# Kernel tuning notes

Measured on AMD Instinct MI355X. Metric: run time of the kernel, lower is better.

The kernel has to match this reference:

```python
import jax, jax.numpy as jnp
import numpy as np

DIM = 96
HEADS = 3
WIN = (8, 8)
B_ = 4096
N = WIN[0] * WIN[1]


def _rel_pos_index(win):
    ch, cw = np.arange(win[0]), np.arange(win[1])
    coords = np.stack(np.meshgrid(ch, cw, indexing='ij'))  # [2, Wh, Ww]
    flat = coords.reshape(2, -1)
    rel = flat[:, :, None] - flat[:, None, :]  # [2, N, N]
    rel = rel.transpose(1, 2, 0).copy()
    rel[:, :, 0] += win[0] - 1
    rel[:, :, 1] += win[1] - 1
    rel[:, :, 0] *= 2 * win[1] - 1
    return jnp.asarray(rel.sum(-1), dtype=jnp.int32)  # [N, N]


def setup_inputs() -> dict:
    key = jax.random.key(0)
    ks = jax.random.split(key, 16)
    C = DIM
    T = (2 * WIN[0] - 1) * (2 * WIN[1] - 1)  # 225
    d = {
        'input_x': jax.random.normal(ks[0], (B_, N, C), jnp.float32),
        'state_x': jax.random.normal(ks[1], (B_, N, C), jnp.float32),
        'Ws': jax.random.normal(ks[2], (4 * C, C), jnp.float32) * 0.02,
        'bs': jnp.zeros((4 * C,), jnp.float32),
        'We': jax.random.normal(ks[3], (4 * C, C), jnp.float32) * 0.02,
        'be': jnp.zeros((4 * C,), jnp.float32),
        'tbl_cv': jax.random.normal(ks[4], (T, HEADS), jnp.float32) * 0.02,
        'tbl_sv': jax.random.normal(ks[5], (T, HEADS), jnp.float32) * 0.02,
        'tbl_ch': jax.random.normal(ks[6], (T, HEADS), jnp.float32) * 0.02,
        'tbl_sh': jax.random.normal(ks[7], (T, HEADS), jnp.float32) * 0.02,
        'Wpv': jax.random.normal(ks[8], (C, 2 * C), jnp.float32) * 0.02,
        'bpv': jnp.zeros((C,), jnp.float32),
        'Wph': jax.random.normal(ks[9], (C, 2 * C), jnp.float32) * 0.02,
        'bph': jnp.zeros((C,), jnp.float32),
        'rel_idx': _rel_pos_index(WIN),
    }
    return d


def _split4(x, W, b, B, n, H, hd):
    # Linear -> [4, B, H, n, hd]
    y = (x @ W.T + b).reshape(B, n, 4, H, hd)
    return jnp.transpose(y, (2, 0, 3, 1, 4))


def reference(input_x, state_x, Ws, bs, We, be, tbl_cv, tbl_sv, tbl_ch, tbl_sh,
              Wpv, bpv, Wph, bph, rel_idx):
    B, n, C = input_x.shape
    H = HEADS
    hd = C // H
    scale = hd ** (-0.5)

    sl = _split4(state_x, Ws, bs, B, n, H, hd)
    el = _split4(input_x, We, be, B, n, H, hd)
    ks_, vs, qsv, qsh = sl[0], sl[1], sl[2], sl[3]
    ke, ve, qev, qeh = el[0], el[1], el[2], el[3]

    def bias(tbl):
        # gather [N,N,H] -> [1,H,N,N]
        return jnp.transpose(tbl[rel_idx], (2, 0, 1))[None]

    # NOTE: faithful to source: self_attn_v is UNscaled, self_attn_h is double-scaled
    attn_cv = jax.nn.softmax(scale * jnp.einsum('bhnd,bhmd->bhnm', qsv, ks_) + bias(tbl_cv), axis=-1)
    attn_sv = jax.nn.softmax(jnp.einsum('bhnd,bhmd->bhnm', qev, ke) + bias(tbl_sv), axis=-1)
    attn_ch = jax.nn.softmax(scale * jnp.einsum('bhnd,bhmd->bhnm', qeh, ke) + bias(tbl_ch), axis=-1)
    attn_sh = jax.nn.softmax((scale * scale) * jnp.einsum('bhnd,bhmd->bhnm', qsh, ks_) + bias(tbl_sh), axis=-1)

    def merge(attn, v):
        return jnp.einsum('bhnm,bhmd->bnhd', attn, v).reshape(B, n, C)

    cross_x_v = merge(attn_cv, vs)
    self_x_v = merge(attn_sv, ve)
    cross_x_h = merge(attn_ch, ve)
    self_x_h = merge(attn_sh, vs)

    out = jnp.concatenate((cross_x_v, self_x_v), axis=2) @ Wpv.T + bpv
    state = jnp.concatenate((cross_x_h, self_x_h), axis=2) @ Wph.T + bph
    return out, state
```

## Files before the change

kernel.cpp:

```cpp
#include <hip/hip_runtime.h>

#define NB 4096
#define NSEQ 64
#define CDIM 96
#define NH 3

typedef __attribute__((ext_vector_type(8))) short bf16x8;
typedef __attribute__((ext_vector_type(4))) float f32x4;
typedef unsigned short u16;

#define MFMA16 __builtin_amdgcn_mfma_f32_16x16x32_bf16

__device__ __forceinline__ u16 f2bf(float f) {
  unsigned u = __builtin_bit_cast(unsigned, f);
  u += 0x7FFFu + ((u >> 16) & 1u);
  return (u16)(u >> 16);
}

__global__ __launch_bounds__(256) void bias_pre_kernel(
    const float* __restrict__ tcv, const float* __restrict__ tsv,
    const float* __restrict__ tch, const float* __restrict__ tsh,
    const int* __restrict__ rel, float* __restrict__ biasF) {
  int idx = blockIdx.x * 256 + threadIdx.x;
  if (idx >= 4 * 3 * 16 * 64) return;
  int t = idx / (3 * 16 * 64);
  int r0 = idx % (3 * 16 * 64);
  int h = r0 / (16 * 64);
  int r1 = r0 % (16 * 64);
  int frag = r1 >> 6;
  int lane = r1 & 63;
  int fr = frag >> 2, fc = frag & 3;
  int g = lane >> 4, q = lane & 15;
  int n = 16 * fc + q;
  int m0 = 16 * fr + 4 * g;
  const float* tbl = (t == 0) ? tcv : (t == 1) ? tsv : (t == 2) ? tch : tsh;
  float4 v;
  v.x = tbl[rel[n * 64 + m0 + 0] * NH + h];
  v.y = tbl[rel[n * 64 + m0 + 1] * NH + h];
  v.z = tbl[rel[n * 64 + m0 + 2] * NH + h];
  v.w = tbl[rel[n * 64 + m0 + 3] * NH + h];
  ((float4*)biasF)[idx] = v;
}

__global__ __launch_bounds__(256) void wcvt_kernel(
    const float* __restrict__ Ws, const float* __restrict__ We,
    const float* __restrict__ Wpv, const float* __restrict__ Wph,
    u16* __restrict__ dst) {
  int i = blockIdx.x * 256 + threadIdx.x;
  if (i >= 110592) return;
  float v;
  if (i < 36864) v = Ws[i];
  else if (i < 73728) v = We[i - 36864];
  else if (i < 92160) v = Wpv[i - 73728];
  else v = Wph[i - 92160];
  dst[i] = f2bf(v);
}

__global__ __launch_bounds__(256, 2) void rwa_kernel(
    const float* __restrict__ Xin, const float* __restrict__ Xst,
    const float* __restrict__ bs, const float* __restrict__ be,
    const float* __restrict__ bpv, const float* __restrict__ bph,
    const float* __restrict__ biasF, const u16* __restrict__ wbf,
    float* __restrict__ out) {
  const int b = blockIdx.x;
  const int t = threadIdx.x;
  const int wu = __builtin_amdgcn_readfirstlane(t >> 6);
  const int lane = t & 63;
  const int g = lane >> 4;
  const int q = lane & 15;

  __shared__ __align__(16) u16 lds[38400];

  const int KS_u = 0, KE_u = 2560, VEt_u = 5120, VSt_u = 7424;
  const int Q_u = 9728 + wu * 2560;
  const int P_u = 19968 + wu * 4608;

  const float SC = 0.17677669529663687f;
  const bool isS = (wu == 0 || wu == 3);
  const float* X = isS ? Xst : Xin;
  const u16* Wt = isS ? (wbf + 0) : (wbf + 36864);
  const float* bt = isS ? bs : be;
  const int qf = (wu < 2) ? 2 : 3;
  const int sf = (wu < 2) ? 0 : 1;
  const int kb_u = (wu == 1 || wu == 2) ? KE_u : KS_u;
  const int vb_u = (wu == 1 || wu == 2) ? VEt_u : VSt_u;
  const int stage_u = (wu == 0) ? KS_u : (wu == 1) ? KE_u : (wu == 2) ? VEt_u : VSt_u;
  const float sc = (wu == 0 || wu == 2) ? SC : ((wu == 1) ? 1.0f : SC * SC);

  const u16* WpvB = wbf + 73728;
  const u16* WphB = wbf + 92160;

  bf16x8 xa[4][3];
#pragma unroll
  for (int fa = 0; fa < 4; fa++) {
    const float* xrow = X + ((size_t)b * NSEQ + 16 * fa + q) * CDIM;
#pragma unroll
    for (int kc = 0; kc < 3; kc++) {
      float xr[8];
      *(float4*)&xr[0] = *(const float4*)(xrow + 32 * kc + 8 * g);
      *(float4*)&xr[4] = *(const float4*)(xrow + 32 * kc + 8 * g + 4);
      bf16x8 v;
#pragma unroll
      for (int j = 0; j < 8; j++) v[j] = (short)f2bf(xr[j]);
      xa[fa][kc] = v;
    }
  }

  f32x4 accO[6], accS[6];
#pragma unroll
  for (int i = 0; i < 6; i++) {
    accO[i] = (f32x4){0.f, 0.f, 0.f, 0.f};
    accS[i] = (f32x4){0.f, 0.f, 0.f, 0.f};
  }

#pragma unroll 1
  for (int h = 0; h < NH; h++) {
    f32x4 pd[4][4];
#pragma unroll
    for (int fa = 0; fa < 4; fa++)
#pragma unroll
      for (int fc = 0; fc < 4; fc++) pd[fa][fc] = (f32x4){0.f, 0.f, 0.f, 0.f};

#pragma unroll
    for (int kc = 0; kc < 3; kc++) {
      bf16x8 bw[4];
#pragma unroll
      for (int fc = 0; fc < 4; fc++) {
        int ch = ((fc < 2) ? qf : sf) * CDIM + h * 32 + (fc & 1) * 16 + q;
        bw[fc] = *(const bf16x8*)&Wt[(size_t)ch * CDIM + 32 * kc + 8 * g];
      }
#pragma unroll
      for (int fa = 0; fa < 4; fa++)
#pragma unroll
        for (int fc = 0; fc < 4; fc++)
          pd[fa][fc] = MFMA16(xa[fa][kc], bw[fc], pd[fa][fc], 0, 0, 0);
    }
    float bq[4];
#pragma unroll
    for (int fc = 0; fc < 4; fc++)
      bq[fc] = bt[((fc < 2) ? qf : sf) * CDIM + h * 32 + (fc & 1) * 16 + q];

#pragma unroll
    for (int fa = 0; fa < 4; fa++) {
#pragma unroll
      for (int fc = 0; fc < 2; fc++)
#pragma unroll
        for (int r = 0; r < 4; r++) {
          int n = 16 * fa + 4 * g + r;
          lds[Q_u + n * 40 + 16 * fc + q] = f2bf(pd[fa][fc][r] + bq[fc]);
        }
      if (wu < 2) {
#pragma unroll
        for (int fc = 2; fc < 4; fc++)
#pragma unroll
          for (int r = 0; r < 4; r++) {
            int n = 16 * fa + 4 * g + r;
            lds[stage_u + n * 40 + 16 * (fc - 2) + q] = f2bf(pd[fa][fc][r] + bq[fc]);
          }
      } else {
#pragma unroll
        for (int fc = 2; fc < 4; fc++) {
          int d = 16 * (fc - 2) + q;
          ushort4 pk;
          pk.x = f2bf(pd[fa][fc][0] + bq[fc]);
          pk.y = f2bf(pd[fa][fc][1] + bq[fc]);
          pk.z = f2bf(pd[fa][fc][2] + bq[fc]);
          pk.w = f2bf(pd[fa][fc][3] + bq[fc]);
          *(ushort4*)&lds[stage_u + d * 72 + 16 * fa + 4 * g] = pk;
        }
      }
    }
    __syncthreads();

    f32x4 lt[4][4];
#pragma unroll
    for (int fr = 0; fr < 4; fr++)
#pragma unroll
      for (int fc = 0; fc < 4; fc++) lt[fr][fc] = (f32x4){0.f, 0.f, 0.f, 0.f};
    bf16x8 ka[4], qb[4];
#pragma unroll
    for (int fr = 0; fr < 4; fr++)
      ka[fr] = *(const bf16x8*)&lds[kb_u + (16 * fr + q) * 40 + 8 * g];
#pragma unroll
    for (int fc = 0; fc < 4; fc++)
      qb[fc] = *(const bf16x8*)&lds[Q_u + (16 * fc + q) * 40 + 8 * g];
#pragma unroll
    for (int fr = 0; fr < 4; fr++)
#pragma unroll
      for (int fc = 0; fc < 4; fc++)
        lt[fr][fc] = MFMA16(ka[fr], qb[fc], lt[fr][fc], 0, 0, 0);

    const float4* bfp = ((const float4*)biasF) + (size_t)((wu * 3 + h) * 16) * 64 + lane;
#pragma unroll
    for (int fr = 0; fr < 4; fr++)
#pragma unroll
      for (int fc = 0; fc < 4; fc++) {
        float4 bv = bfp[(fr * 4 + fc) * 64];
        lt[fr][fc][0] = sc * lt[fr][fc][0] + bv.x;
        lt[fr][fc][1] = sc * lt[fr][fc][1] + bv.y;
        lt[fr][fc][2] = sc * lt[fr][fc][2] + bv.z;
        lt[fr][fc][3] = sc * lt[fr][fc][3] + bv.w;
      }

#pragma unroll
    for (int fc = 0; fc < 4; fc++) {
      float mx = lt[0][fc][0];
#pragma unroll
      for (int fr = 0; fr < 4; fr++)
#pragma unroll
        for (int r = 0; r < 4; r++) mx = fmaxf(mx, lt[fr][fc][r]);
      mx = fmaxf(mx, __shfl_xor(mx, 16));
      mx = fmaxf(mx, __shfl_xor(mx, 32));
      float s = 0.f;
#pragma unroll
      for (int fr = 0; fr < 4; fr++)
#pragma unroll
        for (int r = 0; r < 4; r++) {
          float p = __expf(lt[fr][fc][r] - mx);
          lt[fr][fc][r] = p;
          s += p;
        }
      s += __shfl_xor(s, 16);
      s += __shfl_xor(s, 32);
      float inv = 1.0f / s;
#pragma unroll
      for (int fr = 0; fr < 4; fr++) {
        ushort4 pk;
        pk.x = f2bf(lt[fr][fc][0] * inv);
        pk.y = f2bf(lt[fr][fc][1] * inv);
        pk.z = f2bf(lt[fr][fc][2] * inv);
        pk.w = f2bf(lt[fr][fc][3] * inv);
        *(ushort4*)&lds[P_u + (16 * fc + q) * 72 + 16 * fr + 4 * g] = pk;
      }
    }

    f32x4 ot[2][4];
#pragma unroll
    for (int fa = 0; fa < 2; fa++)
#pragma unroll
      for (int fc = 0; fc < 4; fc++) ot[fa][fc] = (f32x4){0.f, 0.f, 0.f, 0.f};
#pragma unroll
    for (int kc = 0; kc < 2; kc++) {
      bf16x8 va[2], pb[4];
#pragma unroll
      for (int fa = 0; fa < 2; fa++)
        va[fa] = *(const bf16x8*)&lds[vb_u + (16 * fa + q) * 72 + 32 * kc + 8 * g];
#pragma unroll
      for (int fc = 0; fc < 4; fc++)
        pb[fc] = *(const bf16x8*)&lds[P_u + (16 * fc + q) * 72 + 32 * kc + 8 * g];
#pragma unroll
      for (int fa = 0; fa < 2; fa++)
#pragma unroll
        for (int fc = 0; fc < 4; fc++)
          ot[fa][fc] = MFMA16(va[fa], pb[fc], ot[fa][fc], 0, 0, 0);
    }
#pragma unroll
    for (int fa = 0; fa < 2; fa++)
#pragma unroll
      for (int fc = 0; fc < 4; fc++) {
        ushort4 pk;
        pk.x = f2bf(ot[fa][fc][0]);
        pk.y = f2bf(ot[fa][fc][1]);
        pk.z = f2bf(ot[fa][fc][2]);
        pk.w = f2bf(ot[fa][fc][3]);
        *(ushort4*)&lds[P_u + (16 * fc + q) * 40 + 16 * fa + 4 * g] = pk;
      }
    __syncthreads();

    bf16x8 ao[4];
#pragma unroll
    for (int tt = 0; tt < 4; tt++)
      ao[tt] = *(const bf16x8*)&lds[19968 + tt * 4608 + (16 * wu + q) * 40 + 8 * g];
#pragma unroll
    for (int fc = 0; fc < 6; fc++) {
      int c = 16 * fc + q;
      bf16x8 b0 = *(const bf16x8*)&WpvB[(size_t)c * 192 + h * 32 + 8 * g];
      bf16x8 b1 = *(const bf16x8*)&WpvB[(size_t)c * 192 + 96 + h * 32 + 8 * g];
      accO[fc] = MFMA16(ao[0], b0, accO[fc], 0, 0, 0);
      accO[fc] = MFMA16(ao[1], b1, accO[fc], 0, 0, 0);
      bf16x8 b2 = *(const bf16x8*)&WphB[(size_t)c * 192 + h * 32 + 8 * g];
      bf16x8 b3 = *(const bf16x8*)&WphB[(size_t)c * 192 + 96 + h * 32 + 8 * g];
      accS[fc] = MFMA16(ao[2], b2, accS[fc], 0, 0, 0);
      accS[fc] = MFMA16(ao[3], b3, accS[fc], 0, 0, 0);
    }
  }

  float* orow = out + (size_t)b * NSEQ * CDIM;
  float* srow = orow + (size_t)NB * NSEQ * CDIM;
#pragma unroll
  for (int fc = 0; fc < 6; fc++) {
    int c = 16 * fc + q;
    float bo = bpv[c], bh2 = bph[c];
#pragma unroll
    for (int r = 0; r < 4; r++) {
      int n = 16 * wu + 4 * g + r;
      orow[(size_t)n * CDIM + c] = accO[fc][r] + bo;
      srow[(size_t)n * CDIM + c] = accS[fc][r] + bh2;
    }
  }
}

extern "C" void kernel_launch(void* const* d_in, const int* in_sizes, int n_in,
                              void* d_out, int out_size, void* d_ws, size_t ws_size,
                              hipStream_t stream) {
  const float* input_x = (const float*)d_in[0];
  const float* state_x = (const float*)d_in[1];
  const float* Ws   = (const float*)d_in[2];
  const float* bs   = (const float*)d_in[3];
  const float* We   = (const float*)d_in[4];
  const float* be   = (const float*)d_in[5];
  const float* tcv  = (const float*)d_in[6];
  const float* tsv  = (const float*)d_in[7];
  const float* tch  = (const float*)d_in[8];
  const float* tsh  = (const float*)d_in[9];
  const float* Wpv  = (const float*)d_in[10];
  const float* bpv  = (const float*)d_in[11];
  const float* Wph  = (const float*)d_in[12];
  const float* bph  = (const float*)d_in[13];
  const int*   rel  = (const int*)d_in[14];

  float* biasF = (float*)d_ws;
  u16* wbf = (u16*)((char*)d_ws + 196608);

  bias_pre_kernel<<<48, 256, 0, stream>>>(tcv, tsv, tch, tsh, rel, biasF);
  wcvt_kernel<<<432, 256, 0, stream>>>(Ws, We, Wpv, Wph, wbf);
  rwa_kernel<<<NB, 256, 0, stream>>>(input_x, state_x, bs, be, bpv, bph,
                                     biasF, wbf, (float*)d_out);
}
```

Measured before the change: 633.7 us.

## Shrink LDS footprint, swizzle P/V layout, and use packed bf16 conversion with exp2 softmax

Shared memory is cut by merging each wave's Q and P staging into one reused region, and launch bounds rise from 2 to 3 blocks per CU. The P and V^T tiles use an XOR-swizzled 64-wide layout to avoid LDS bank conflicts. The projection MFMAs are reordered so results land in vectorized 4-element row segments. Scalar f32-to-bf16 rounding is replaced by the hardware v_cvt_pk_bf16_f32 instruction. The softmax scale and log2(e) are folded into Q and the bias so exp2 can be used, and normalization is deferred to the PV output. An extra barrier protects the reused region, and the higher occupancy target may force register spilling.

```diff
diff --git a/kernel.cpp b/kernel.cpp
--- a/kernel.cpp
+++ b/kernel.cpp
@@ -10,11 +10,12 @@
 typedef unsigned short u16;
 
 #define MFMA16 __builtin_amdgcn_mfma_f32_16x16x32_bf16
-
-__device__ __forceinline__ u16 f2bf(float f) {
-  unsigned u = __builtin_bit_cast(unsigned, f);
-  u += 0x7FFFu + ((u >> 16) & 1u);
-  return (u16)(u >> 16);
+#define LOG2E 1.4426950408889634f
+
+__device__ __forceinline__ unsigned pkbf(float a, float b) {
+  unsigned r;
+  asm("v_cvt_pk_bf16_f32 %0, %1, %2" : "=v"(r) : "v"(a), "v"(b));
+  return r;
 }
 
 __global__ __launch_bounds__(256) void bias_pre_kernel(
@@ -35,10 +36,10 @@
   int m0 = 16 * fr + 4 * g;
   const float* tbl = (t == 0) ? tcv : (t == 1) ? tsv : (t == 2) ? tch : tsh;
   float4 v;
-  v.x = tbl[rel[n * 64 + m0 + 0] * NH + h];
-  v.y = tbl[rel[n * 64 + m0 + 1] * NH + h];
-  v.z = tbl[rel[n * 64 + m0 + 2] * NH + h];
-  v.w = tbl[rel[n * 64 + m0 + 3] * NH + h];
+  v.x = LOG2E * tbl[rel[n * 64 + m0 + 0] * NH + h];
+  v.y = LOG2E * tbl[rel[n * 64 + m0 + 1] * NH + h];
+  v.z = LOG2E * tbl[rel[n * 64 + m0 + 2] * NH + h];
+  v.w = LOG2E * tbl[rel[n * 64 + m0 + 3] * NH + h];
   ((float4*)biasF)[idx] = v;
 }
 
@@ -53,10 +54,12 @@
   else if (i < 73728) v = We[i - 36864];
   else if (i < 92160) v = Wpv[i - 73728];
   else v = Wph[i - 92160];
-  dst[i] = f2bf(v);
-}
-
-__global__ __launch_bounds__(256, 2) void rwa_kernel(
+  unsigned u = __builtin_bit_cast(unsigned, v);
+  u += 0x7FFFu + ((u >> 16) & 1u);
+  dst[i] = (u16)(u >> 16);
+}
+
+__global__ __launch_bounds__(256, 3) void rwa_kernel(
     const float* __restrict__ Xin, const float* __restrict__ Xst,
     const float* __restrict__ bs, const float* __restrict__ be,
     const float* __restrict__ bpv, const float* __restrict__ bph,
@@ -69,23 +72,22 @@
   const int g = lane >> 4;
   const int q = lane & 15;
 
-  __shared__ __align__(16) u16 lds[38400];
-
-  const int KS_u = 0, KE_u = 2560, VEt_u = 5120, VSt_u = 7424;
-  const int Q_u = 9728 + wu * 2560;
-  const int P_u = 19968 + wu * 4608;
+  __shared__ __align__(16) u16 lds[25600];
+
+  const int KS_u = 0, KE_u = 2560, VST_u = 5120, VET_u = 7168;
+  const int PW_u = 9216 + wu * 4096;
 
   const float SC = 0.17677669529663687f;
   const bool isS = (wu == 0 || wu == 3);
   const float* X = isS ? Xst : Xin;
-  const u16* Wt = isS ? (wbf + 0) : (wbf + 36864);
+  const u16* Wt = isS ? wbf : (wbf + 36864);
   const float* bt = isS ? bs : be;
   const int qf = (wu < 2) ? 2 : 3;
   const int sf = (wu < 2) ? 0 : 1;
   const int kb_u = (wu == 1 || wu == 2) ? KE_u : KS_u;
-  const int vb_u = (wu == 1 || wu == 2) ? VEt_u : VSt_u;
-  const int stage_u = (wu == 0) ? KS_u : (wu == 1) ? KE_u : (wu == 2) ? VEt_u : VSt_u;
-  const float sc = (wu == 0 || wu == 2) ? SC : ((wu == 1) ? 1.0f : SC * SC);
+  const int vb_u = (wu == 1 || wu == 2) ? VET_u : VST_u;
+  const int stage_u = (wu == 0) ? KS_u : (wu == 1) ? KE_u : (wu == 2) ? VET_u : VST_u;
+  const float scl = ((wu == 0 || wu == 2) ? SC : ((wu == 1) ? 1.0f : SC * SC)) * LOG2E;
 
   const u16* WpvB = wbf + 73728;
   const u16* WphB = wbf + 92160;
@@ -96,13 +98,14 @@
     const float* xrow = X + ((size_t)b * NSEQ + 16 * fa + q) * CDIM;
 #pragma unroll
     for (int kc = 0; kc < 3; kc++) {
-      float xr[8];
-      *(float4*)&xr[0] = *(const float4*)(xrow + 32 * kc + 8 * g);
-      *(float4*)&xr[4] = *(const float4*)(xrow + 32 * kc + 8 * g + 4);
-      bf16x8 v;
-#pragma unroll
-      for (int j = 0; j < 8; j++) v[j] = (short)f2bf(xr[j]);
-      xa[fa][kc] = v;
+      float4 lo = *(const float4*)(xrow + 32 * kc + 8 * g);
+      float4 hi = *(const float4*)(xrow + 32 * kc + 8 * g + 4);
+      union { bf16x8 v; unsigned u[4]; } tmp;
+      tmp.u[0] = pkbf(lo.x, lo.y);
+      tmp.u[1] = pkbf(lo.z, lo.w);
+      tmp.u[2] = pkbf(hi.x, hi.y);
+      tmp.u[3] = pkbf(hi.z, hi.w);
+      xa[fa][kc] = tmp.v;
     }
   }
 
@@ -115,60 +118,110 @@
 
 #pragma unroll 1
   for (int h = 0; h < NH; h++) {
-    f32x4 pd[4][4];
-#pragma unroll
-    for (int fa = 0; fa < 4; fa++)
-#pragma unroll
-      for (int fc = 0; fc < 4; fc++) pd[fa][fc] = (f32x4){0.f, 0.f, 0.f, 0.f};
-
-#pragma unroll
-    for (int kc = 0; kc < 3; kc++) {
-      bf16x8 bw[4];
-#pragma unroll
-      for (int fc = 0; fc < 4; fc++) {
-        int ch = ((fc < 2) ? qf : sf) * CDIM + h * 32 + (fc & 1) * 16 + q;
-        bw[fc] = *(const bf16x8*)&Wt[(size_t)ch * CDIM + 32 * kc + 8 * g];
-      }
+    const int qbase = qf * CDIM + h * 32;
+    const int sbase = sf * CDIM + h * 32;
+
+    if (wu < 2) {
+      f32x4 pq[2][4], pk2[2][4];
+#pragma unroll
+      for (int cb = 0; cb < 2; cb++)
+#pragma unroll
+        for (int nb = 0; nb < 4; nb++) {
+          pq[cb][nb] = (f32x4){0.f, 0.f, 0.f, 0.f};
+          pk2[cb][nb] = (f32x4){0.f, 0.f, 0.f, 0.f};
+        }
+#pragma unroll
+      for (int kc = 0; kc < 3; kc++) {
+        bf16x8 wq[2], wk[2];
+#pragma unroll
+        for (int cb = 0; cb < 2; cb++) {
+          wq[cb] = *(const bf16x8*)&Wt[(size_t)(qbase + 16 * cb + q) * CDIM + 32 * kc + 8 * g];
+          wk[cb] = *(const bf16x8*)&Wt[(size_t)(sbase + 16 * cb + q) * CDIM + 32 * kc + 8 * g];
+        }
+#pragma unroll
+        for (int cb = 0; cb < 2; cb++)
+#pragma unroll
+          for (int nb = 0; nb < 4; nb++) {
+            pq[cb][nb] = MFMA16(wq[cb], xa[nb][kc], pq[cb][nb], 0, 0, 0);
+            pk2[cb][nb] = MFMA16(wk[cb], xa[nb][kc], pk2[cb][nb], 0, 0, 0);
+          }
+      }
+#pragma unroll
+      for (int cb = 0; cb < 2; cb++) {
+        float4 bq = *(const float4*)&bt[qbase + 16 * cb + 4 * g];
+        float4 bk = *(const float4*)&bt[sbase + 16 * cb + 4 * g];
+#pragma unroll
+        for (int nb = 0; nb < 4; nb++) {
+          int n = 16 * nb + q;
+          f32x4 v = pq[cb][nb];
+          uint2 w2;
+          w2.x = pkbf((v[0] + bq.x) * scl, (v[1] + bq.y) * scl);
+          w2.y = pkbf((v[2] + bq.z) * scl, (v[3] + bq.w) * scl);
+          *(uint2*)&lds[PW_u + n * 40 + 16 * cb + 4 * g] = w2;
+          f32x4 u = pk2[cb][nb];
+          uint2 k2;
+          k2.x = pkbf(u[0] + bk.x, u[1] + bk.y);
+          k2.y = pkbf(u[2] + bk.z, u[3] + bk.w);
+          *(uint2*)&lds[stage_u + n * 40 + 16 * cb + 4 * g] = k2;
+        }
+      }
+    } else {
+      f32x4 pq[2][4], pv[4][2];
+#pragma unroll
+      for (int cb = 0; cb < 2; cb++)
+#pragma unroll
+        for (int nb = 0; nb < 4; nb++) pq[cb][nb] = (f32x4){0.f, 0.f, 0.f, 0.f};
 #pragma unroll
       for (int fa = 0; fa < 4; fa++)
 #pragma unroll
-        for (int fc = 0; fc < 4; fc++)
-          pd[fa][fc] = MFMA16(xa[fa][kc], bw[fc], pd[fa][fc], 0, 0, 0);
-    }
-    float bq[4];
-#pragma unroll
-    for (int fc = 0; fc < 4; fc++)
-      bq[fc] = bt[((fc < 2) ? qf : sf) * CDIM + h * 32 + (fc & 1) * 16 + q];
-
-#pragma unroll
-    for (int fa = 0; fa < 4; fa++) {
-#pragma unroll
-      for (int fc = 0; fc < 2; fc++)
-#pragma unroll
-        for (int r = 0; r < 4; r++) {
-          int n = 16 * fa + 4 * g + r;
-          lds[Q_u + n * 40 + 16 * fc + q] = f2bf(pd[fa][fc][r] + bq[fc]);
-        }
-      if (wu < 2) {
-#pragma unroll
-        for (int fc = 2; fc < 4; fc++)
-#pragma unroll
-          for (int r = 0; r < 4; r++) {
-            int n = 16 * fa + 4 * g + r;
-            lds[stage_u + n * 40 + 16 * (fc - 2) + q] = f2bf(pd[fa][fc][r] + bq[fc]);
-          }
-      } else {
-#pragma unroll
-        for (int fc = 2; fc < 4; fc++) {
-          int d = 16 * (fc - 2) + q;
-          ushort4 pk;
-          pk.x = f2bf(pd[fa][fc][0] + bq[fc]);
-          pk.y = f2bf(pd[fa][fc][1] + bq[fc]);
-          pk.z = f2bf(pd[fa][fc][2] + bq[fc]);
-          pk.w = f2bf(pd[fa][fc][3] + bq[fc]);
-          *(ushort4*)&lds[stage_u + d * 72 + 16 * fa + 4 * g] = pk;
-        }
-      }
+        for (int fc = 0; fc < 2; fc++) pv[fa][fc] = (f32x4){0.f, 0.f, 0.f, 0.f};
+#pragma unroll
+      for (int kc = 0; kc < 3; kc++) {
+        bf16x8 wq[2], wv[2];
+#pragma unroll
+        for (int cb = 0; cb < 2; cb++)
+          wq[cb] = *(const bf16x8*)&Wt[(size_t)(qbase + 16 * cb + q) * CDIM + 32 * kc + 8 * g];
+#pragma unroll
+        for (int fc = 0; fc < 2; fc++)
+          wv[fc] = *(const bf16x8*)&Wt[(size_t)(sbase + 16 * fc + q) * CDIM + 32 * kc + 8 * g];
+#pragma unroll
+        for (int cb = 0; cb < 2; cb++)
+#pragma unroll
+          for (int nb = 0; nb < 4; nb++)
+            pq[cb][nb] = MFMA16(wq[cb], xa[nb][kc], pq[cb][nb], 0, 0, 0);
+#pragma unroll
+        for (int fa = 0; fa < 4; fa++)
+#pragma unroll
+          for (int fc = 0; fc < 2; fc++)
+            pv[fa][fc] = MFMA16(xa[fa][kc], wv[fc], pv[fa][fc], 0, 0, 0);
+      }
+#pragma unroll
+      for (int cb = 0; cb < 2; cb++) {
+        float4 bq = *(const float4*)&bt[qbase + 16 * cb + 4 * g];
+#pragma unroll
+        for (int nb = 0; nb < 4; nb++) {
+          int n = 16 * nb + q;
+          f32x4 v = pq[cb][nb];
+          uint2 w2;
+          w2.x = pkbf((v[0] + bq.x) * scl, (v[1] + bq.y) * scl);
+          w2.y = pkbf((v[2] + bq.z) * scl, (v[3] + bq.w) * scl);
+          *(uint2*)&lds[PW_u + n * 40 + 16 * cb + 4 * g] = w2;
+        }
+      }
+      float bv0 = bt[sbase + q], bv1 = bt[sbase + 16 + q];
+#pragma unroll
+      for (int fa = 0; fa < 4; fa++)
+#pragma unroll
+        for (int fc = 0; fc < 2; fc++) {
+          int d = 16 * fc + q;
+          float bvv = fc ? bv1 : bv0;
+          f32x4 v = pv[fa][fc];
+          uint2 w2;
+          w2.x = pkbf(v[0] + bvv, v[1] + bvv);
+          w2.y = pkbf(v[2] + bvv, v[3] + bvv);
+          int idx = ((d << 6) + 16 * fa + 4 * g) ^ ((d & 7) << 3);
+          *(uint2*)&lds[stage_u + idx] = w2;
+        }
     }
     __syncthreads();
 
@@ -183,7 +236,7 @@
       ka[fr] = *(const bf16x8*)&lds[kb_u + (16 * fr + q) * 40 + 8 * g];
 #pragma unroll
     for (int fc = 0; fc < 4; fc++)
-      qb[fc] = *(const bf16x8*)&lds[Q_u + (16 * fc + q) * 40 + 8 * g];
+      qb[fc] = *(const bf16x8*)&lds[PW_u + (16 * fc + q) * 40 + 8 * g];
 #pragma unroll
     for (int fr = 0; fr < 4; fr++)
 #pragma unroll
@@ -196,12 +249,13 @@
 #pragma unroll
       for (int fc = 0; fc < 4; fc++) {
         float4 bv = bfp[(fr * 4 + fc) * 64];
-        lt[fr][fc][0] = sc * lt[fr][fc][0] + bv.x;
-        lt[fr][fc][1] = sc * lt[fr][fc][1] + bv.y;
-        lt[fr][fc][2] = sc * lt[fr][fc][2] + bv.z;
-        lt[fr][fc][3] = sc * lt[fr][fc][3] + bv.w;
-      }
-
+        lt[fr][fc][0] += bv.x;
+        lt[fr][fc][1] += bv.y;
+        lt[fr][fc][2] += bv.z;
+        lt[fr][fc][3] += bv.w;
+      }
+
+    float inv4[4];
 #pragma unroll
     for (int fc = 0; fc < 4; fc++) {
       float mx = lt[0][fc][0];
@@ -216,21 +270,21 @@
       for (int fr = 0; fr < 4; fr++)
 #pragma unroll
         for (int r = 0; r < 4; r++) {
-          float p = __expf(lt[fr][fc][r] - mx);
+          float p = __builtin_exp2f(lt[fr][fc][r] - mx);
           lt[fr][fc][r] = p;
           s += p;
         }
       s += __shfl_xor(s, 16);
       s += __shfl_xor(s, 32);
-      float inv = 1.0f / s;
+      inv4[fc] = 1.0f / s;
+      int n = 16 * fc + q;
 #pragma unroll
       for (int fr = 0; fr < 4; fr++) {
-        ushort4 pk;
-        pk.x = f2bf(lt[fr][fc][0] * inv);
-        pk.y = f2bf(lt[fr][fc][1] * inv);
-        pk.z = f2bf(lt[fr][fc][2] * inv);
-        pk.w = f2bf(lt[fr][fc][3] * inv);
-        *(ushort4*)&lds[P_u + (16 * fc + q) * 72 + 16 * fr + 4 * g] = pk;
+        uint2 w2;
+        w2.x = pkbf(lt[fr][fc][0], lt[fr][fc][1]);
+        w2.y = pkbf(lt[fr][fc][2], lt[fr][fc][3]);
+        int idx = ((n << 6) + 16 * fr + 4 * g) ^ ((n & 7) << 3);
+        *(uint2*)&lds[PW_u + idx] = w2;
       }
     }
 
@@ -243,11 +297,15 @@
     for (int kc = 0; kc < 2; kc++) {
       bf16x8 va[2], pb[4];
 #pragma unroll
-      for (int fa = 0; fa < 2; fa++)
-        va[fa] = *(const bf16x8*)&lds[vb_u + (16 * fa + q) * 72 + 32 * kc + 8 * g];
-#pragma unroll
-      for (int fc = 0; fc < 4; fc++)
-        pb[fc] = *(const bf16x8*)&lds[P_u + (16 * fc + q) * 72 + 32 * kc + 8 * g];
+      for (int fa = 0; fa < 2; fa++) {
+        int d = 16 * fa + q;
+        va[fa] = *(const bf16x8*)&lds[vb_u + (((d << 6) + 32 * kc + 8 * g) ^ ((d & 7) << 3))];
+      }
+#pragma unroll
+      for (int fc = 0; fc < 4; fc++) {
+        int n = 16 * fc + q;
+        pb[fc] = *(const bf16x8*)&lds[PW_u + (((n << 6) + 32 * kc + 8 * g) ^ ((n & 7) << 3))];
+      }
 #pragma unroll
       for (int fa = 0; fa < 2; fa++)
 #pragma unroll
@@ -258,19 +316,20 @@
     for (int fa = 0; fa < 2; fa++)
 #pragma unroll
       for (int fc = 0; fc < 4; fc++) {
-        ushort4 pk;
-        pk.x = f2bf(ot[fa][fc][0]);
-        pk.y = f2bf(ot[fa][fc][1]);
-        pk.z = f2bf(ot[fa][fc][2]);
-        pk.w = f2bf(ot[fa][fc][3]);
-        *(ushort4*)&lds[P_u + (16 * fc + q) * 40 + 16 * fa + 4 * g] = pk;
+        float iv = inv4[fc];
+        int n = 16 * fc + q;
+        uint2 w2;
+        w2.x = pkbf(ot[fa][fc][0] * iv, ot[fa][fc][1] * iv);
+        w2.y = pkbf(ot[fa][fc][2] * iv, ot[fa][fc][3] * iv);
+        *(uint2*)&lds[PW_u + n * 40 + 16 * fa + 4 * g] = w2;
       }
     __syncthreads();
 
     bf16x8 ao[4];
 #pragma unroll
     for (int tt = 0; tt < 4; tt++)
-      ao[tt] = *(const bf16x8*)&lds[19968 + tt * 4608 + (16 * wu + q) * 40 + 8 * g];
+      ao[tt] = *(const bf16x8*)&lds[9216 + tt * 4096 + (16 * wu + q) * 40 + 8 * g];
+    if (h < NH - 1) __syncthreads();
 #pragma unroll
     for (int fc = 0; fc < 6; fc++) {
       int c = 16 * fc + q;
```

New measurement: 1.011 ms. 1.6x slower.
